# Kernel optimization log

Measured on AMD Instinct MI355X. Metric: run time of the kernel, lower is better.

## Reference

```python
import jax, jax.numpy as jnp
import numpy as np

N_HIDDEN = 128
N_HEAD = 8
DIM_HEAD = N_HIDDEN // N_HEAD


def setup_inputs() -> dict:
    key = jax.random.key(0)
    ks = jax.random.split(key, 16)
    B, N, H = 2, 512, N_HIDDEN
    x = jax.random.normal(ks[0], (B, N, H), dtype=jnp.float32)
    e = jax.random.normal(ks[1], (B, N, N, H), dtype=jnp.float32)
    attention_mask = jnp.zeros((B, 1, N, N), dtype=jnp.float32)
    s = 1.0 / np.sqrt(H)
    def lin(kw, kb):
        W = jax.random.normal(kw, (H, H), dtype=jnp.float32) * s
        b = jax.random.normal(kb, (H,), dtype=jnp.float32) * s
        return W, b
    Wq, bq = lin(ks[2], ks[3])
    Wk, bk = lin(ks[4], ks[5])
    We, be = lin(ks[6], ks[7])
    Woh, boh = lin(ks[8], ks[9])
    Woe, boe = lin(ks[10], ks[11])
    return {"x": x, "e": e, "attention_mask": attention_mask,
            "Wq": Wq, "bq": bq, "Wk": Wk, "bk": bk,
            "We": We, "be": be, "Woh": Woh, "boh": boh,
            "Woe": Woe, "boe": boe}


def reference(x, e, attention_mask, Wq, bq, Wk, bk, We, be, Woh, boh, Woe, boe):
    B, N, H = x.shape
    h, dh = N_HEAD, DIM_HEAD
    # Projections -> [B, h, N, dh]
    Qx = (x @ Wq + bq).reshape(B, N, h, dh).transpose(0, 2, 1, 3)
    Kx = (x @ Wk + bk).reshape(B, N, h, dh).transpose(0, 2, 1, 3)
    Vx = Kx  # faithful to original: V_x = self.K(x)
    # Edge projection -> [B, h, N, N, dh]
    Ee = (e @ We + be).reshape(B, N, N, h, dh).transpose(0, 3, 1, 2, 4)
    # Elementwise Q*K*E biased scores: [B, h, N, N, dh]
    inter = Qx[:, :, :, None, :] * Kx[:, :, None, :, :] * Ee / np.sqrt(dh).astype(np.float32)
    scores = jax.nn.softmax(attention_mask + inter.sum(-1), axis=-1)  # [B, h, N, N]
    # Edge output: [B, N, N, H] -> Oe (dropout is identity at eval)
    e_out = inter.transpose(0, 2, 3, 1, 4).reshape(B, N, N, H) @ Woe + boe
    # Node output
    att = jnp.einsum('bhij,bhjd->bhid', scores, Vx)  # [B, h, N, dh]
    x_out = att.transpose(0, 2, 1, 3).reshape(B, N, H) @ Woh + boh
    return (x_out, e_out, scores)
```

## Files before the change

### kernel.cpp

```cpp
#include <hip/hip_runtime.h>
#include <hip/hip_bf16.h>


#define NB 2
#define NN 512
#define NHID 128
#define BQ 32

typedef __bf16 bf16x8 __attribute__((ext_vector_type(8)));
typedef float  f32x4  __attribute__((ext_vector_type(4)));

union U16 { uint4 u; bf16x8 v; };

__global__ __launch_bounds__(128)
void proj_kernel(const float* __restrict__ x,
                 const float* __restrict__ Wq, const float* __restrict__ bq,
                 const float* __restrict__ Wk, const float* __restrict__ bk,
                 float* __restrict__ Qhat, float* __restrict__ Khat)
{
    const int row = blockIdx.x;
    const int c   = threadIdx.x;
    __shared__ float xs[NHID];
    xs[c] = x[(long)row*NHID + c];
    __syncthreads();
    float q = bq[c], k = bk[c];
    #pragma unroll 8
    for (int kk = 0; kk < NHID; ++kk) {
        const float xv = xs[kk];
        q += xv * Wq[kk*NHID + c];
        k += xv * Wk[kk*NHID + c];
    }
    Qhat[(long)row*NHID + c] = q;
    Khat[(long)row*NHID + c] = k;
}

__global__ __launch_bounds__(128)
void wcvt_kernel(const float* __restrict__ We, const float* __restrict__ Woe,
                 __bf16* __restrict__ WeT, __bf16* __restrict__ WoeT)
{
    const int cb = blockIdx.x;
    const int k  = threadIdx.x;
    if (cb < NHID) {
        WeT[cb*NHID + k] = (__bf16)We[k*NHID + cb];
    } else {
        const int c = cb - NHID;
        WoeT[c*NHID + k] = (__bf16)Woe[k*NHID + c];
    }
}

__global__ __launch_bounds__(256, 2)
void mha_main(const float* __restrict__ e,
              const float* __restrict__ mask,
              const float* __restrict__ be,
              const float* __restrict__ boe,
              const float* __restrict__ Woh,
              const float* __restrict__ boh,
              const float* __restrict__ Qhat,
              const float* __restrict__ Khat,
              const __bf16* __restrict__ WeT,
              const __bf16* __restrict__ WoeT,
              float* __restrict__ xout,
              float* __restrict__ eout,
              float* __restrict__ sout)
{
    const int i   = blockIdx.x;
    const int b   = blockIdx.y;
    const int tid = threadIdx.x;
    const int w   = tid >> 6;
    const int l   = tid & 63;
    const int l15 = l & 15;
    const int lg  = l >> 4;
    const int wcol = w * 32;

    __shared__ __align__(16) float  Elds[2][BQ*NHID];
    __shared__ __align__(16) __bf16 Mlds[BQ*NHID];
    __shared__ float Llog[8][NN];
    __shared__ float AttP[2][NHID];
    __shared__ float AttF[NHID];

    const long rowbi = (long)b*NN + i;
    const float* Esrc = e    + rowbi*(long)(NN*NHID);
    float*       Edst = eout + rowbi*(long)(NN*NHID);
    const float* Kb   = Khat + (long)b*NN*NHID;

    float qv[2], bev[2], boev[2];
    bf16x8 fWe[2][4], fWoe[2][4];
    #pragma unroll
    for (int ct = 0; ct < 2; ++ct) {
        const int c = wcol + ct*16 + l15;
        qv[ct]   = Qhat[rowbi*NHID + c] * 0.25f;
        bev[ct]  = be[c];
        boev[ct] = boe[c];
        #pragma unroll
        for (int ks = 0; ks < 4; ++ks) {
            const int kb = ks*32 + lg*8;
            U16 ua, ub;
            ua.u = *(const uint4*)(WeT  + c*NHID + kb);
            ub.u = *(const uint4*)(WoeT + c*NHID + kb);
            fWe[ct][ks]  = ua.v;
            fWoe[ct][ks] = ub.v;
        }
    }

    float4 rf[4];
    {
        const float4* src = (const float4*)Esrc;
        #pragma unroll
        for (int it = 0; it < 4; ++it) rf[it] = src[it*256 + tid];
        #pragma unroll
        for (int it = 0; it < 4; ++it) {
            const int L = (it*256 + tid)*4;
            const int row = L >> 7, k = L & 127;
            *(float4*)&Elds[0][row*NHID + (k ^ ((row&7)<<2))] = rf[it];
        }
    }

    for (int t = 0; t < 16; ++t) {
        const int cur = t & 1;
        if (t < 15) {
            const float4* src = (const float4*)(Esrc + (long)(t+1)*(BQ*NHID));
            #pragma unroll
            for (int it = 0; it < 4; ++it) rf[it] = src[it*256 + tid];
        }
        __syncthreads();

        f32x4 acc1[2][2] = {};
        #pragma unroll
        for (int ks = 0; ks < 4; ++ks) {
            bf16x8 fa[2];
            #pragma unroll
            for (int rt = 0; rt < 2; ++rt) {
                const int row = rt*16 + l15;
                const int kb  = ks*32 + lg*8;
                const int sw  = (row & 7) << 2;
                const float* bp = &Elds[cur][row*NHID];
                const float4 a0 = *(const float4*)(bp + ((kb    ) ^ sw));
                const float4 a1 = *(const float4*)(bp + ((kb + 4) ^ sw));
                bf16x8 v;
                v[0]=(__bf16)a0.x; v[1]=(__bf16)a0.y; v[2]=(__bf16)a0.z; v[3]=(__bf16)a0.w;
                v[4]=(__bf16)a1.x; v[5]=(__bf16)a1.y; v[6]=(__bf16)a1.z; v[7]=(__bf16)a1.w;
                fa[rt] = v;
            }
            #pragma unroll
            for (int rt = 0; rt < 2; ++rt)
                #pragma unroll
                for (int ct = 0; ct < 2; ++ct)
                    acc1[rt][ct] = __builtin_amdgcn_mfma_f32_16x16x32_bf16(
                        fa[rt], fWe[ct][ks], acc1[rt][ct], 0, 0, 0);
        }

        #pragma unroll
        for (int rt = 0; rt < 2; ++rt) {
            #pragma unroll
            for (int ct = 0; ct < 2; ++ct) {
                const int c = wcol + ct*16 + l15;
                #pragma unroll
                for (int rg = 0; rg < 4; ++rg) {
                    const int jl = rt*16 + lg*4 + rg;
                    const float ee  = acc1[rt][ct][rg] + bev[ct];
                    const float kvv = Kb[(long)(t*BQ + jl)*NHID + c];
                    const float m   = ee * qv[ct] * kvv;
                    Mlds[jl*NHID + (c ^ ((jl&7)<<3))] = (__bf16)m;
                    float s = m;
                    s += __shfl_xor(s, 1);
                    s += __shfl_xor(s, 2);
                    s += __shfl_xor(s, 4);
                    s += __shfl_xor(s, 8);
                    if (l15 == 0) Llog[w*2 + ct][t*BQ + jl] = s;
                }
            }
        }

        if (t < 15) {
            #pragma unroll
            for (int it = 0; it < 4; ++it) {
                const int L = (it*256 + tid)*4;
                const int row = L >> 7, k = L & 127;
                *(float4*)&Elds[1-cur][row*NHID + (k ^ ((row&7)<<2))] = rf[it];
            }
        }
        __syncthreads();

        f32x4 acc2[2][2] = {};
        #pragma unroll
        for (int ks = 0; ks < 4; ++ks) {
            bf16x8 fa[2];
            #pragma unroll
            for (int rt = 0; rt < 2; ++rt) {
                const int row = rt*16 + l15;
                const int kb  = ks*32 + lg*8;
                U16 u;
                u.u = *(const uint4*)&Mlds[row*NHID + (kb ^ ((row&7)<<3))];
                fa[rt] = u.v;
            }
            #pragma unroll
            for (int rt = 0; rt < 2; ++rt)
                #pragma unroll
                for (int ct = 0; ct < 2; ++ct)
                    acc2[rt][ct] = __builtin_amdgcn_mfma_f32_16x16x32_bf16(
                        fa[rt], fWoe[ct][ks], acc2[rt][ct], 0, 0, 0);
        }
        #pragma unroll
        for (int rt = 0; rt < 2; ++rt)
            #pragma unroll
            for (int ct = 0; ct < 2; ++ct) {
                const int c = wcol + ct*16 + l15;
                #pragma unroll
                for (int rg = 0; rg < 4; ++rg) {
                    const int jl = rt*16 + lg*4 + rg;
                    Edst[(long)(t*BQ + jl)*NHID + c] = acc2[rt][ct][rg] + boev[ct];
                }
            }
    }
    __syncthreads();

    const float* mrow = mask + rowbi*NN;
    #pragma unroll
    for (int hh = 0; hh < 2; ++hh) {
        const int h = w*2 + hh;
        float vb[8];
        float mx = -1e30f;
        #pragma unroll
        for (int q = 0; q < 8; ++q) {
            const int j = q*64 + l;
            const float v = Llog[h][j] + mrow[j];
            vb[q] = v; mx = fmaxf(mx, v);
        }
        #pragma unroll
        for (int mm = 1; mm < 64; mm <<= 1) mx = fmaxf(mx, __shfl_xor(mx, mm));
        float sum = 0.f;
        #pragma unroll
        for (int q = 0; q < 8; ++q) { vb[q] = __expf(vb[q] - mx); sum += vb[q]; }
        #pragma unroll
        for (int mm = 1; mm < 64; mm <<= 1) sum += __shfl_xor(sum, mm);
        const float inv = 1.f / sum;
        float* srow = sout + ((long)(b*8 + h)*NN + i)*NN;
        #pragma unroll
        for (int q = 0; q < 8; ++q) {
            const int j = q*64 + l;
            const float p = vb[q]*inv;
            Llog[h][j] = p;
            srow[j] = p;
        }
    }
    __syncthreads();

    {
        const int half = tid >> 7;
        const int c = tid & 127;
        const int h = c >> 4;
        float a = 0.f;
        const float* kp = Kb + (long)(half*256)*NHID + c;
        const float* pp = &Llog[h][half*256];
        #pragma unroll 4
        for (int j = 0; j < 256; ++j) a += pp[j] * kp[(long)j*NHID];
        AttP[half][c] = a;
    }
    __syncthreads();
    if (tid < NHID) AttF[tid] = AttP[0][tid] + AttP[1][tid];
    __syncthreads();

    if (tid < NHID) {
        const int c = tid;
        float acc = boh[c];
        #pragma unroll 8
        for (int k = 0; k < NHID; ++k) acc += AttF[k] * Woh[k*NHID + c];
        xout[rowbi*NHID + c] = acc;
    }
}

extern "C" void kernel_launch(void* const* d_in, const int* in_sizes, int n_in,
                              void* d_out, int out_size, void* d_ws, size_t ws_size,
                              hipStream_t stream) {
    const float* x    = (const float*)d_in[0];
    const float* e    = (const float*)d_in[1];
    const float* mask = (const float*)d_in[2];
    const float* Wq   = (const float*)d_in[3];
    const float* bq   = (const float*)d_in[4];
    const float* Wk   = (const float*)d_in[5];
    const float* bk   = (const float*)d_in[6];
    const float* We   = (const float*)d_in[7];
    const float* be   = (const float*)d_in[8];
    const float* Woh  = (const float*)d_in[9];
    const float* boh  = (const float*)d_in[10];
    const float* Woe  = (const float*)d_in[11];
    const float* boe  = (const float*)d_in[12];

    float*  Qhat = (float*)d_ws;
    float*  Khat = Qhat + NB*NN*NHID;
    __bf16* WeT  = (__bf16*)(Khat + NB*NN*NHID);
    __bf16* WoeT = WeT + NHID*NHID;

    float* xout = (float*)d_out;
    float* eout = xout + (long)NB*NN*NHID;
    float* sout = eout + (long)NB*NN*NN*NHID;

    proj_kernel<<<dim3(NB*NN), 128, 0, stream>>>(x, Wq, bq, Wk, bk, Qhat, Khat);
    wcvt_kernel<<<dim3(2*NHID), 128, 0, stream>>>(We, Woe, WeT, WoeT);
    mha_main<<<dim3(NN, NB), 256, 0, stream>>>(e, mask, be, boe, Woh, boh,
                                               Qhat, Khat, WeT, WoeT,
                                               xout, eout, sout);
}
```

Before: 304.7 us.

## Stage edge tiles as bf16 in LDS, compute head sums via MFMA, raise occupancy

The staged edge tile in shared memory now holds bf16 instead of fp32. This halves that LDS footprint, removes the per-use conversion, and allows the launch bound to go from 2 to 3 blocks per SM. The per-head score sums are computed by one wave with extra MFMAs against a 0/1 selector matrix, replacing the shuffle reductions. K values are preloaded into registers before the loop. The final dot products are split into several independent accumulators. The MFMA head sums read the bf16-rounded products, which adds some rounding error to the scores. Tighter register limits may also cause spills.

```diff
diff --git a/kernel.cpp b/kernel.cpp
--- a/kernel.cpp
+++ b/kernel.cpp
@@ -8,6 +8,7 @@
 #define BQ 32
 
 typedef __bf16 bf16x8 __attribute__((ext_vector_type(8)));
+typedef __bf16 bf16x4 __attribute__((ext_vector_type(4)));
 typedef float  f32x4  __attribute__((ext_vector_type(4)));
 
 union U16 { uint4 u; bf16x8 v; };
@@ -48,7 +49,7 @@
     }
 }
 
-__global__ __launch_bounds__(256, 2)
+__global__ __launch_bounds__(256, 3)
 void mha_main(const float* __restrict__ e,
               const float* __restrict__ mask,
               const float* __restrict__ be,
@@ -72,7 +73,7 @@
     const int lg  = l >> 4;
     const int wcol = w * 32;
 
-    __shared__ __align__(16) float  Elds[2][BQ*NHID];
+    __shared__ __align__(16) __bf16 Elds[2][BQ*NHID];
     __shared__ __align__(16) __bf16 Mlds[BQ*NHID];
     __shared__ float Llog[8][NN];
     __shared__ float AttP[2][NHID];
@@ -101,6 +102,8 @@
             fWoe[ct][ks] = ub.v;
         }
     }
+    const bool selp[4] = { (0*2 + (lg>>1)) == l15, (1*2 + (lg>>1)) == l15,
+                           (2*2 + (lg>>1)) == l15, (3*2 + (lg>>1)) == l15 };
 
     float4 rf[4];
     {
@@ -111,12 +114,24 @@
         for (int it = 0; it < 4; ++it) {
             const int L = (it*256 + tid)*4;
             const int row = L >> 7, k = L & 127;
-            *(float4*)&Elds[0][row*NHID + (k ^ ((row&7)<<2))] = rf[it];
+            bf16x4 v;
+            v[0]=(__bf16)rf[it].x; v[1]=(__bf16)rf[it].y;
+            v[2]=(__bf16)rf[it].z; v[3]=(__bf16)rf[it].w;
+            *(bf16x4*)&Elds[0][row*NHID + (k ^ ((row&7)<<3))] = v;
         }
     }
 
     for (int t = 0; t < 16; ++t) {
         const int cur = t & 1;
+        float kreg[2][2][4];
+        #pragma unroll
+        for (int rt = 0; rt < 2; ++rt)
+            #pragma unroll
+            for (int ct = 0; ct < 2; ++ct)
+                #pragma unroll
+                for (int rg = 0; rg < 4; ++rg)
+                    kreg[rt][ct][rg] =
+                        Kb[(long)(t*BQ + rt*16 + lg*4 + rg)*NHID + wcol + ct*16 + l15];
         if (t < 15) {
             const float4* src = (const float4*)(Esrc + (long)(t+1)*(BQ*NHID));
             #pragma unroll
@@ -131,15 +146,7 @@
             #pragma unroll
             for (int rt = 0; rt < 2; ++rt) {
                 const int row = rt*16 + l15;
-                const int kb  = ks*32 + lg*8;
-                const int sw  = (row & 7) << 2;
-                const float* bp = &Elds[cur][row*NHID];
-                const float4 a0 = *(const float4*)(bp + ((kb    ) ^ sw));
-                const float4 a1 = *(const float4*)(bp + ((kb + 4) ^ sw));
-                bf16x8 v;
-                v[0]=(__bf16)a0.x; v[1]=(__bf16)a0.y; v[2]=(__bf16)a0.z; v[3]=(__bf16)a0.w;
-                v[4]=(__bf16)a1.x; v[5]=(__bf16)a1.y; v[6]=(__bf16)a1.z; v[7]=(__bf16)a1.w;
-                fa[rt] = v;
+                fa[rt] = *(const bf16x8*)&Elds[cur][row*NHID + ((ks*32 + lg*8) ^ ((row&7)<<3))];
             }
             #pragma unroll
             for (int rt = 0; rt < 2; ++rt)
@@ -150,48 +157,41 @@
         }
 
         #pragma unroll
-        for (int rt = 0; rt < 2; ++rt) {
+        for (int rt = 0; rt < 2; ++rt)
             #pragma unroll
             for (int ct = 0; ct < 2; ++ct) {
                 const int c = wcol + ct*16 + l15;
                 #pragma unroll
                 for (int rg = 0; rg < 4; ++rg) {
                     const int jl = rt*16 + lg*4 + rg;
-                    const float ee  = acc1[rt][ct][rg] + bev[ct];
-                    const float kvv = Kb[(long)(t*BQ + jl)*NHID + c];
-                    const float m   = ee * qv[ct] * kvv;
+                    const float ee = acc1[rt][ct][rg] + bev[ct];
+                    const float m  = ee * qv[ct] * kreg[rt][ct][rg];
                     Mlds[jl*NHID + (c ^ ((jl&7)<<3))] = (__bf16)m;
-                    float s = m;
-                    s += __shfl_xor(s, 1);
-                    s += __shfl_xor(s, 2);
-                    s += __shfl_xor(s, 4);
-                    s += __shfl_xor(s, 8);
-                    if (l15 == 0) Llog[w*2 + ct][t*BQ + jl] = s;
                 }
             }
-        }
 
         if (t < 15) {
             #pragma unroll
             for (int it = 0; it < 4; ++it) {
                 const int L = (it*256 + tid)*4;
                 const int row = L >> 7, k = L & 127;
-                *(float4*)&Elds[1-cur][row*NHID + (k ^ ((row&7)<<2))] = rf[it];
+                bf16x4 v;
+                v[0]=(__bf16)rf[it].x; v[1]=(__bf16)rf[it].y;
+                v[2]=(__bf16)rf[it].z; v[3]=(__bf16)rf[it].w;
+                *(bf16x4*)&Elds[1-cur][row*NHID + (k ^ ((row&7)<<3))] = v;
             }
         }
         __syncthreads();
 
         f32x4 acc2[2][2] = {};
+        f32x4 accL[2] = {};
         #pragma unroll
         for (int ks = 0; ks < 4; ++ks) {
             bf16x8 fa[2];
             #pragma unroll
             for (int rt = 0; rt < 2; ++rt) {
                 const int row = rt*16 + l15;
-                const int kb  = ks*32 + lg*8;
-                U16 u;
-                u.u = *(const uint4*)&Mlds[row*NHID + (kb ^ ((row&7)<<3))];
-                fa[rt] = u.v;
+                fa[rt] = *(const bf16x8*)&Mlds[row*NHID + ((ks*32 + lg*8) ^ ((row&7)<<3))];
             }
             #pragma unroll
             for (int rt = 0; rt < 2; ++rt)
@@ -199,6 +199,16 @@
                 for (int ct = 0; ct < 2; ++ct)
                     acc2[rt][ct] = __builtin_amdgcn_mfma_f32_16x16x32_bf16(
                         fa[rt], fWoe[ct][ks], acc2[rt][ct], 0, 0, 0);
+            if (w == 0) {
+                U16 us;
+                const unsigned ones = 0x3f803f80u;
+                us.u.x = selp[ks] ? ones : 0u;
+                us.u.y = us.u.x; us.u.z = us.u.x; us.u.w = us.u.x;
+                #pragma unroll
+                for (int rt = 0; rt < 2; ++rt)
+                    accL[rt] = __builtin_amdgcn_mfma_f32_16x16x32_bf16(
+                        fa[rt], us.v, accL[rt], 0, 0, 0);
+            }
         }
         #pragma unroll
         for (int rt = 0; rt < 2; ++rt)
@@ -211,6 +221,13 @@
                     Edst[(long)(t*BQ + jl)*NHID + c] = acc2[rt][ct][rg] + boev[ct];
                 }
             }
+        if (w == 0 && l15 < 8) {
+            #pragma unroll
+            for (int rt = 0; rt < 2; ++rt)
+                #pragma unroll
+                for (int rg = 0; rg < 4; ++rg)
+                    Llog[l15][t*BQ + rt*16 + lg*4 + rg] = accL[rt][rg];
+        }
     }
     __syncthreads();
 
@@ -249,12 +266,17 @@
         const int half = tid >> 7;
         const int c = tid & 127;
         const int h = c >> 4;
-        float a = 0.f;
+        float a0 = 0.f, a1 = 0.f, a2 = 0.f, a3 = 0.f;
         const float* kp = Kb + (long)(half*256)*NHID + c;
         const float* pp = &Llog[h][half*256];
         #pragma unroll 4
-        for (int j = 0; j < 256; ++j) a += pp[j] * kp[(long)j*NHID];
-        AttP[half][c] = a;
+        for (int j = 0; j < 256; j += 4) {
+            a0 += pp[j]   * kp[(long)(j  )*NHID];
+            a1 += pp[j+1] * kp[(long)(j+1)*NHID];
+            a2 += pp[j+2] * kp[(long)(j+2)*NHID];
+            a3 += pp[j+3] * kp[(long)(j+3)*NHID];
+        }
+        AttP[half][c] = (a0 + a1) + (a2 + a3);
     }
     __syncthreads();
     if (tid < NHID) AttF[tid] = AttP[0][tid] + AttP[1][tid];
@@ -262,10 +284,13 @@
 
     if (tid < NHID) {
         const int c = tid;
-        float acc = boh[c];
+        float a0 = boh[c], a1 = 0.f;
         #pragma unroll 8
-        for (int k = 0; k < NHID; ++k) acc += AttF[k] * Woh[k*NHID + c];
-        xout[rowbi*NHID + c] = acc;
+        for (int k = 0; k < NHID; k += 2) {
+            a0 += AttF[k]   * Woh[(k  )*NHID + c];
+            a1 += AttF[k+1] * Woh[(k+1)*NHID + c];
+        }
+        xout[rowbi*NHID + c] = a0 + a1;
     }
 }
 
```

New measurement: 372.8 us. 22.4% more time.
